# Performance work log

Hardware: AMD Instinct MI355X
Metric: run time of the kernel (lower is better)

The kernel has to match this reference:

```python
import jax, jax.numpy as jnp
import numpy as np

D = 256       # d_model
HEADS = 8     # n_heads
PTS = 4       # n_points
FF = 1024     # dim_feedforward
HD = D // HEADS
B, Q = 8, 900
HH, WW = 100, 100


def setup_inputs() -> dict:
    key = jax.random.key(0)
    ks = iter(jax.random.split(key, 40))
    p = lambda shape: jax.random.normal(next(ks), shape, dtype=jnp.float32) * 0.02
    inp = {
        "tgt": jax.random.normal(next(ks), (B, Q, D), dtype=jnp.float32),
        "memory": jax.random.normal(next(ks), (B, HH * WW, D), dtype=jnp.float32),
        "H": HH,
        "W": WW,
        # self-attention (nn.MultiheadAttention) params
        "in_proj_w": p((3 * D, D)), "in_proj_b": p((3 * D,)),
        "out_proj_w": p((D, D)), "out_proj_b": p((D,)),
        # layer norms
        "norm1_s": jnp.ones((D,)), "norm1_b": jnp.zeros((D,)),
        "norm2_s": jnp.ones((D,)), "norm2_b": jnp.zeros((D,)),
        "norm3_s": jnp.ones((D,)), "norm3_b": jnp.zeros((D,)),
        # deformable cross-attention params
        "vproj_w": p((D, D)), "vproj_b": p((D,)),
        "offs_w": p((HEADS * PTS * 2, D)), "offs_b": p((HEADS * PTS * 2,)),
        "attw_w": p((HEADS * PTS, D)), "attw_b": p((HEADS * PTS,)),
        "ref_w": p((2, D)), "ref_b": p((2,)),
        "cout_w": p((D, D)), "cout_b": p((D,)),
        # FFN params
        "ffn_w1": p((FF, D)), "ffn_b1": p((FF,)),
        "ffn_w2": p((D, FF)), "ffn_b2": p((D,)),
    }
    return inp


def _layer_norm(x, s, b):
    m = jnp.mean(x, -1, keepdims=True)
    v = jnp.mean((x - m) ** 2, -1, keepdims=True)
    return (x - m) * jax.lax.rsqrt(v + 1e-5) * s + b


def _mha(x, wi, bi, wo, bo):
    b, q, _ = x.shape
    qkv = x @ wi.T + bi
    qh, kh, vh = jnp.split(qkv, 3, axis=-1)
    qh = qh.reshape(b, q, HEADS, HD).transpose(0, 2, 1, 3)
    kh = kh.reshape(b, q, HEADS, HD).transpose(0, 2, 1, 3)
    vh = vh.reshape(b, q, HEADS, HD).transpose(0, 2, 1, 3)
    att = jax.nn.softmax(jnp.einsum('bhqd,bhkd->bhqk', qh, kh) / np.float32(np.sqrt(HD)), axis=-1)
    o = jnp.einsum('bhqk,bhkd->bhqd', att, vh).transpose(0, 2, 1, 3).reshape(b, q, D)
    return o @ wo.T + bo


def _deform_attn(q, mem, H, W, vproj_w, vproj_b, offs_w, offs_b, attw_w, attw_b,
                 ref_w, ref_b, cout_w, cout_b):
    b, nq, _ = q.shape
    # per-query normalized reference points (x, y) in [0,1]
    ref = jax.nn.sigmoid(q @ ref_w.T + ref_b)                         # [B,Q,2]
    offs = (q @ offs_w.T + offs_b).reshape(b, nq, HEADS, PTS, 2)      # [B,Q,h,p,2]
    attw = jax.nn.softmax((q @ attw_w.T + attw_b).reshape(b, nq, HEADS, PTS), axis=-1)
    val = (mem @ vproj_w.T + vproj_b).reshape(b, H * W, HEADS, HD).transpose(0, 2, 1, 3)  # [B,h,HW,hd]
    wh = jnp.array([W, H], dtype=q.dtype)
    loc = ref[:, :, None, None, :] + offs / wh                        # normalized sampling loc
    x = loc[..., 0] * W - 0.5                                         # pixel coords (align_corners=False)
    y = loc[..., 1] * H - 0.5
    x0 = jnp.floor(x); y0 = jnp.floor(y)
    lx = x - x0; ly = y - y0
    x0i = x0.astype(jnp.int32); y0i = y0.astype(jnp.int32)

    def gather(xi, yi):
        valid = ((xi >= 0) & (xi < W) & (yi >= 0) & (yi < H)).astype(q.dtype)
        idx = jnp.clip(yi, 0, H - 1) * W + jnp.clip(xi, 0, W - 1)     # [B,Q,h,p]
        idxt = idx.transpose(0, 2, 1, 3).reshape(b, HEADS, nq * PTS, 1)
        g = jnp.take_along_axis(val, idxt, axis=2)                    # [B,h,Q*p,hd]
        g = g.reshape(b, HEADS, nq, PTS, HD).transpose(0, 2, 1, 3, 4)  # [B,Q,h,p,hd]
        return g * valid[..., None]

    samp = (gather(x0i, y0i) * ((1 - lx) * (1 - ly))[..., None]
            + gather(x0i + 1, y0i) * (lx * (1 - ly))[..., None]
            + gather(x0i, y0i + 1) * ((1 - lx) * ly)[..., None]
            + gather(x0i + 1, y0i + 1) * (lx * ly)[..., None])        # [B,Q,h,p,hd]
    out = jnp.sum(samp * attw[..., None], axis=3).reshape(b, nq, D)
    return out @ cout_w.T + cout_b


def reference(tgt, memory, H, W, in_proj_w, in_proj_b, out_proj_w, out_proj_b,
              norm1_s, norm1_b, norm2_s, norm2_b, norm3_s, norm3_b,
              vproj_w, vproj_b, offs_w, offs_b, attw_w, attw_b, ref_w, ref_b,
              cout_w, cout_b, ffn_w1, ffn_b1, ffn_w2, ffn_b2):
    t2 = _mha(tgt, in_proj_w, in_proj_b, out_proj_w, out_proj_b)
    t = _layer_norm(tgt + t2, norm1_s, norm1_b)
    t2 = _deform_attn(t, memory, H, W, vproj_w, vproj_b, offs_w, offs_b,
                      attw_w, attw_b, ref_w, ref_b, cout_w, cout_b)
    t = _layer_norm(t + t2, norm2_s, norm2_b)
    f = jnp.maximum(t @ ffn_w1.T + ffn_b1, 0) @ ffn_w2.T + ffn_b2
    return _layer_norm(t + f, norm3_s, norm3_b)
```

## Files before the change

### kernel.cpp

```cpp
#include <hip/hip_runtime.h>
#include <hip/hip_bf16.h>

typedef __hip_bfloat16 bf16;
typedef __attribute__((ext_vector_type(8))) short short8;
typedef __attribute__((ext_vector_type(4))) float f32x4;

#define BB 8
#define QQ 900
#define DD 256
#define NH 8
#define HD 32
#define NPTS 4
#define FFD 1024
#define HH 100
#define WW2 100
#define HWTOT 10000

#define QT 64
#define KTC 128
#define NCHUNK ((QQ + KTC - 1) / KTC)
#define QB 4
#define VTP 1024

__device__ inline float tofloat(float x) { return x; }
__device__ inline float tofloat(bf16 x) { return __bfloat162float(x); }
__device__ inline float bf2f(unsigned short u) {
    return __uint_as_float(((unsigned int)u) << 16);
}
__device__ inline void storev(bf16* p, float v) { *p = __float2bfloat16(v); }
__device__ inline void storev(float* p, float v) { *p = v; }

__device__ inline void load4(const float* p, float* v) {
    const float4 t = *(const float4*)p;
    v[0] = t.x; v[1] = t.y; v[2] = t.z; v[3] = t.w;
}
__device__ inline void load4(const bf16* p, float* v) {
    const ushort4 t = *(const ushort4*)p;
    v[0] = bf2f(t.x); v[1] = bf2f(t.y); v[2] = bf2f(t.z); v[3] = bf2f(t.w);
}
__device__ inline void store4(float* p, const float* v) {
    float4 t = {v[0], v[1], v[2], v[3]};
    *(float4*)p = t;
}
__device__ inline void store4(bf16* p, const float* v) {
    bf16 t[4] = {__float2bfloat16(v[0]), __float2bfloat16(v[1]),
                 __float2bfloat16(v[2]), __float2bfloat16(v[3])};
    *(uint2*)p = *(const uint2*)t;
}
__device__ inline void cvt4(const float* s, bf16* d) {
    float v[4];
    load4(s, v);
    store4(d, v);
}

typedef __attribute__((address_space(1))) const unsigned int gas_u32;
typedef __attribute__((address_space(3))) unsigned int las_u32;
__device__ inline void gload_lds16(const bf16* g, bf16* l) {
    __builtin_amdgcn_global_load_lds(
        (gas_u32*)(unsigned long long)(const void*)g,
        (las_u32*)(unsigned int)(unsigned long long)(const void*)l, 16, 0, 0);
}

__global__ void pack_kernel(const float* __restrict__ in_proj_w, const float* __restrict__ out_proj_w,
                            const float* __restrict__ cout_w, const float* __restrict__ ffn_w1,
                            const float* __restrict__ ffn_w2, const float* __restrict__ vproj_w,
                            const float* __restrict__ offs_w, const float* __restrict__ attw_w,
                            const float* __restrict__ ref_w, const float* __restrict__ offs_b,
                            const float* __restrict__ attw_b, const float* __restrict__ ref_b,
                            const float* __restrict__ tgt, bf16* __restrict__ wpk,
                            bf16* __restrict__ tgtb, float* __restrict__ dbias,
                            bf16* __restrict__ vt) {
    const int i4 = (blockIdx.x * 256 + threadIdx.x) * 4;
    const int TOT = 950272 + 1843200 + 128 + 2097152;
    if (i4 >= TOT) return;
    if (i4 < 196608) {
        cvt4(in_proj_w + i4, wpk + i4);
    } else if (i4 < 262144) {
        cvt4(out_proj_w + (i4 - 196608), wpk + i4);
    } else if (i4 < 327680) {
        cvt4(cout_w + (i4 - 262144), wpk + i4);
    } else if (i4 < 589824) {
        cvt4(ffn_w1 + (i4 - 327680), wpk + i4);
    } else if (i4 < 851968) {
        cvt4(ffn_w2 + (i4 - 589824), wpk + i4);
    } else if (i4 < 917504) {
        cvt4(vproj_w + (i4 - 851968), wpk + i4);
    } else if (i4 < 950272) {
#pragma unroll
        for (int j = 0; j < 4; ++j) {
            const int jj = i4 + j - 917504;
            const int r = jj >> 8, c = jj & 255;
            float v = 0.f;
            if (r < 64) v = offs_w[r * 256 + c];
            else if (r < 96) v = attw_w[(r - 64) * 256 + c];
            else if (r < 98) v = ref_w[(r - 96) * 256 + c];
            wpk[i4 + j] = __float2bfloat16(v);
        }
    } else if (i4 < 950272 + 1843200) {
        cvt4(tgt + (i4 - 950272), tgtb + (i4 - 950272));
    } else if (i4 < 950272 + 1843200 + 128) {
#pragma unroll
        for (int j = 0; j < 4; ++j) {
            const int jj = i4 + j - (950272 + 1843200);
            float v = 0.f;
            if (jj < 64) v = offs_b[jj];
            else if (jj < 96) v = attw_b[jj - 64];
            else if (jj < 98) v = ref_b[jj - 96];
            dbias[jj] = v;
        }
    } else {
        const uint2 z = {0u, 0u};
        *(uint2*)&vt[i4 - (950272 + 1843200 + 128)] = z;
    }
}

template <int BM, int BN, int BK, int ACT, int VT, typename OT>
__global__ __launch_bounds__(256) void gemm_v6(const bf16* __restrict__ A,
                                               const bf16* __restrict__ W,
                                               const float* __restrict__ bias,
                                               OT* __restrict__ C, bf16* __restrict__ vt,
                                               int M, int N, int K) {
    constexpr int MACC = BM / 32;
    constexpr int NACC = BN / 32;
    constexpr int KK = BK / 32;
    constexpr int P = BK / 8;
    constexpr int CA = (BM * BK) / 8 / 256;
    constexpr int CB = (BN * BK) / 8 / 256;
    __shared__ bf16 As[2][BM * BK];
    __shared__ bf16 Bs[2][BN * BK];
    const int bm = blockIdx.y * BM, bn = blockIdx.x * BN;
    const int tid = threadIdx.x;
    const int lane = tid & 63, wave = tid >> 6;
    const int l15 = lane & 15, g = lane >> 4;
    const int wr = wave & 1, wc = wave >> 1;
    auto swz = [](int row) { return (P == 8) ? (row & 7) : ((row >> 1) & 3); };
    const f32x4 zf = {0.f, 0.f, 0.f, 0.f};
    f32x4 acc[MACC][NACC];
#pragma unroll
    for (int mi = 0; mi < MACC; ++mi)
#pragma unroll
        for (int ni = 0; ni < NACC; ++ni) acc[mi][ni] = zf;

    const int NT = K / BK;
    int cur = 0;

    {
#pragma unroll
        for (int i = 0; i < CA; ++i) {
            const int slot = i * 256 + wave * 64 + lane;
            const int row = slot / P, pc = slot % P;
            const int gp = pc ^ swz(row);
            const int grow = min(bm + row, M - 1);
            gload_lds16(A + (size_t)grow * K + 0 + gp * 8,
                        &As[0][(i * 256 + wave * 64) * 8]);
        }
#pragma unroll
        for (int i = 0; i < CB; ++i) {
            const int slot = i * 256 + wave * 64 + lane;
            const int row = slot / P, pc = slot % P;
            const int gp = pc ^ swz(row);
            gload_lds16(W + (size_t)(bn + row) * K + 0 + gp * 8,
                        &Bs[0][(i * 256 + wave * 64) * 8]);
        }
    }
    __syncthreads();

    for (int t = 0; t < NT; ++t) {
        if (t + 1 < NT) {
            const int k0 = (t + 1) * BK;
#pragma unroll
            for (int i = 0; i < CA; ++i) {
                const int slot = i * 256 + wave * 64 + lane;
                const int row = slot / P, pc = slot % P;
                const int gp = pc ^ swz(row);
                const int grow = min(bm + row, M - 1);
                gload_lds16(A + (size_t)grow * K + k0 + gp * 8,
                            &As[cur ^ 1][(i * 256 + wave * 64) * 8]);
            }
#pragma unroll
            for (int i = 0; i < CB; ++i) {
                const int slot = i * 256 + wave * 64 + lane;
                const int row = slot / P, pc = slot % P;
                const int gp = pc ^ swz(row);
                gload_lds16(W + (size_t)(bn + row) * K + k0 + gp * 8,
                            &Bs[cur ^ 1][(i * 256 + wave * 64) * 8]);
            }
        }
#pragma unroll
        for (int kk = 0; kk < KK; ++kk) {
            short8 af[MACC];
#pragma unroll
            for (int mi = 0; mi < MACC; ++mi) {
                const int row = wr * (BM / 2) + mi * 16 + l15;
                const int byte = row * (2 * BK) + (((kk * 4 + g) ^ swz(row)) << 4);
                af[mi] = *(const short8*)((const char*)&As[cur][0] + byte);
            }
#pragma unroll
            for (int ni = 0; ni < NACC; ++ni) {
                const int col = wc * (BN / 2) + ni * 16 + l15;
                const int byte = col * (2 * BK) + (((kk * 4 + g) ^ swz(col)) << 4);
                const short8 bfv = *(const short8*)((const char*)&Bs[cur][0] + byte);
#pragma unroll
                for (int mi = 0; mi < MACC; ++mi)
                    acc[mi][ni] = __builtin_amdgcn_mfma_f32_16x16x32_bf16(af[mi], bfv,
                                                                          acc[mi][ni], 0, 0, 0);
            }
        }
        __syncthreads();
        cur ^= 1;
    }

#pragma unroll
    for (int ni = 0; ni < NACC; ++ni) {
        const int col = bn + wc * (BN / 2) + ni * 16 + l15;
        const float bv = bias[col];
#pragma unroll
        for (int mi = 0; mi < MACC; ++mi) {
            const int row0 = bm + wr * (BM / 2) + mi * 16 + g * 4;
            if (VT && col >= 512) {
                if (row0 < M) {
                    const int b = row0 / 900, q = row0 % 900;
                    const int hd = col - 512;
                    bf16 u4[4];
#pragma unroll
                    for (int r = 0; r < 4; ++r) u4[r] = __float2bfloat16(acc[mi][ni][r] + bv);
                    *(uint2*)&vt[((size_t)(b * NH + (hd >> 5)) * HD + (hd & 31)) * VTP + q] =
                        *(const uint2*)u4;
                }
            } else {
#pragma unroll
                for (int r = 0; r < 4; ++r) {
                    const int row = row0 + r;
                    if (row < M) {
                        float v = acc[mi][ni][r] + bv;
                        if (ACT == 1) v = fmaxf(v, 0.f);
                        if (VT)
                            storev((bf16*)C + (size_t)row * 512 + col, v);
                        else
                            storev(&C[(size_t)row * N + col], v);
                    }
                }
            }
        }
    }
}

__global__ __launch_bounds__(256) void mha_mfma_kernel(const bf16* __restrict__ qkv,
                                                       const bf16* __restrict__ vt,
                                                       bf16* __restrict__ o) {
    const int qt = blockIdx.x, h = blockIdx.y, b = blockIdx.z;
    const int tid = threadIdx.x;
    const int lane = tid & 63, wave = tid >> 6;
    const int l15 = lane & 15, g = lane >> 4;
    __shared__ bf16 KP[4096];
    __shared__ bf16 Vls[4096];
    __shared__ bf16 Pls[4][16][136];
    const size_t base = (size_t)b * QQ * 512;
    const bf16* vbase = vt + (size_t)(b * NH + h) * HD * VTP;
    const int q0 = qt * QT;

    short8 qa = {0, 0, 0, 0, 0, 0, 0, 0};
    {
        const int qg = q0 + wave * 16 + l15;
        if (qg < QQ)
            qa = *(const short8*)(qkv + base + (size_t)qg * 512 + h * HD + g * 8);
    }
    f32x4 accO[2] = {{0.f, 0.f, 0.f, 0.f}, {0.f, 0.f, 0.f, 0.f}};
    float l_acc[4] = {0.f, 0.f, 0.f, 0.f};
    const float sl2e = 0.17677669529663687f * 1.4426950408889634f;

    for (int c = 0; c < NCHUNK; ++c) {
        const int k0 = c * KTC;
        __syncthreads();
#pragma unroll
        for (int i = 0; i < 2; ++i) {
            const int r = (wave * 2 + i) * 16 + (lane >> 2);
            const int p = lane & 3;
            const int gp = p ^ ((r >> 1) & 3);
            const int kg = min(k0 + r, QQ - 1);
            gload_lds16(qkv + base + (size_t)kg * 512 + 256 + h * HD + gp * 8,
                        &KP[(wave * 2 + i) * 512]);
        }
#pragma unroll
        for (int i = 0; i < 2; ++i) {
            const int s = (wave * 2 + i) * 64 + lane;
            const int vrow = s >> 4, vp = s & 15;
            const int gp = vp ^ (vrow & 7);
            gload_lds16(vbase + (size_t)vrow * VTP + k0 + gp * 8, &Vls[(wave * 2 + i) * 512]);
        }
        __syncthreads();

        f32x4 s[8];
#pragma unroll
        for (int t = 0; t < 8; ++t) {
            const int row = t * 16 + l15;
            const short8 kb = *(const short8*)&KP[row * 32 + (g ^ ((row >> 1) & 3)) * 8];
            const f32x4 z = {0.f, 0.f, 0.f, 0.f};
            s[t] = __builtin_amdgcn_mfma_f32_16x16x32_bf16(qa, kb, z, 0, 0, 0);
        }
#pragma unroll
        for (int t = 0; t < 8; ++t) {
            const bool cv = (k0 + t * 16 + l15) < QQ;
#pragma unroll
            for (int r = 0; r < 4; ++r) {
                const float p = cv ? exp2f(s[t][r] * sl2e) : 0.f;
                l_acc[r] += p;
                Pls[wave][g * 4 + r][t * 16 + l15] = __float2bfloat16(p);
            }
        }
#pragma unroll
        for (int s4 = 0; s4 < 4; ++s4) {
            const short8 pa = *(const short8*)&Pls[wave][l15][s4 * 32 + g * 8];
#pragma unroll
            for (int t2 = 0; t2 < 2; ++t2) {
                const int vrow = t2 * 16 + l15;
                const int pp = (s4 * 4 + g) ^ (vrow & 7);
                const short8 vb = *(const short8*)&Vls[vrow * 128 + pp * 8];
                accO[t2] = __builtin_amdgcn_mfma_f32_16x16x32_bf16(pa, vb, accO[t2], 0, 0, 0);
            }
        }
    }
#pragma unroll
    for (int r = 0; r < 4; ++r) {
        float l = l_acc[r];
        l += __shfl_xor(l, 1);
        l += __shfl_xor(l, 2);
        l += __shfl_xor(l, 4);
        l += __shfl_xor(l, 8);
        const int row = q0 + wave * 16 + g * 4 + r;
        if (row < QQ) {
            const float inv = 1.f / l;
#pragma unroll
            for (int t2 = 0; t2 < 2; ++t2) {
                storev(&o[((size_t)b * QQ + row) * DD + h * HD + t2 * 16 + l15],
                       accO[t2][r] * inv);
            }
        }
    }
}

template <typename TR, typename TO>
__global__ __launch_bounds__(256) void add_ln_kernel(const TR* __restrict__ resid,
                                                     const bf16* __restrict__ y,
                                                     const float* __restrict__ g,
                                                     const float* __restrict__ bta,
                                                     TO* __restrict__ out) {
    const int tid = threadIdx.x;
    const int lane = tid & 63, wave = tid >> 6;
    const int row = blockIdx.x * 4 + wave;
    const int c0 = lane * 4;
    const size_t base = (size_t)row * DD + c0;
    float v[4], yv[4];
    load4(resid + base, v);
    load4(y + base, yv);
#pragma unroll
    for (int j = 0; j < 4; ++j) v[j] += yv[j];
    float s = v[0] + v[1] + v[2] + v[3];
    s += __shfl_xor(s, 1);  s += __shfl_xor(s, 2);  s += __shfl_xor(s, 4);
    s += __shfl_xor(s, 8);  s += __shfl_xor(s, 16); s += __shfl_xor(s, 32);
    const float mean = s * (1.f / DD);
    float d[4];
    float q = 0.f;
#pragma unroll
    for (int j = 0; j < 4; ++j) {
        d[j] = v[j] - mean;
        q += d[j] * d[j];
    }
    q += __shfl_xor(q, 1);  q += __shfl_xor(q, 2);  q += __shfl_xor(q, 4);
    q += __shfl_xor(q, 8);  q += __shfl_xor(q, 16); q += __shfl_xor(q, 32);
    const float rstd = rsqrtf(q * (1.f / DD) + 1e-5f);
    float gv[4], bv[4], ov[4];
    load4(g + c0, gv);
    load4(bta + c0, bv);
#pragma unroll
    for (int j = 0; j < 4; ++j) ov[j] = d[j] * rstd * gv[j] + bv[j];
    store4(out + base, ov);
}

__global__ __launch_bounds__(256) void deform_gather_kernel(
    const float* __restrict__ dots, const float* __restrict__ mem,
    bf16* __restrict__ G, float* __restrict__ wsumg) {
    const int qt = blockIdx.x, b = blockIdx.y;
    const int tid = threadIdx.x;
    const int q0 = qt * QB;
    __shared__ int sidx[QB][32][4];
    __shared__ float swt[QB][32][4];

    if (tid < 128) {
        const int q = tid >> 5, hp = tid & 31;
        const float* dr = dots + ((size_t)b * QQ + q0 + q) * 128;
        const float ox = dr[hp * 2], oy = dr[hp * 2 + 1];
        float ad = dr[64 + hp];
        const float rx = dr[96], ry = dr[97];
        float mx = ad;
        mx = fmaxf(mx, __shfl_xor(mx, 1));
        mx = fmaxf(mx, __shfl_xor(mx, 2));
        float e = __expf(ad - mx);
        float sm = e;
        sm += __shfl_xor(sm, 1);
        sm += __shfl_xor(sm, 2);
        const float a = e / sm;
        const float refx = 1.f / (1.f + __expf(-rx));
        const float refy = 1.f / (1.f + __expf(-ry));
        const float x = (refx + ox * (1.f / WW2)) * WW2 - 0.5f;
        const float y = (refy + oy * (1.f / HH)) * HH - 0.5f;
        const float x0f = floorf(x), y0f = floorf(y);
        const float lx = x - x0f, ly = y - y0f;
        const int x0 = (int)x0f, y0 = (int)y0f;
        const float cw[4] = {(1 - lx) * (1 - ly), lx * (1 - ly), (1 - lx) * ly, lx * ly};
        const int cx[4] = {x0, x0 + 1, x0, x0 + 1};
        const int cy[4] = {y0, y0, y0 + 1, y0 + 1};
        float cs = 0.f;
#pragma unroll
        for (int cc = 0; cc < 4; ++cc) {
            const bool valid = cx[cc] >= 0 && cx[cc] < WW2 && cy[cc] >= 0 && cy[cc] < HH;
            const int xi = min(max(cx[cc], 0), WW2 - 1);
            const int yi = min(max(cy[cc], 0), HH - 1);
            sidx[q][hp][cc] = yi * WW2 + xi;
            const float w = valid ? a * cw[cc] : 0.f;
            swt[q][hp][cc] = w;
            cs += w;
        }
        cs += __shfl_xor(cs, 1);
        cs += __shfl_xor(cs, 2);
        if ((hp & 3) == 0) wsumg[((size_t)b * QQ + q0 + q) * NH + (hp >> 2)] = cs;
    }
    __syncthreads();

    {
        const int q = tid >> 6, cbase = (tid & 63) * 4;
        const float* mb = mem + (size_t)b * HWTOT * DD;
        bf16* gq = G + ((size_t)(b * QQ + q0 + q) * NH) * DD + cbase;
#pragma unroll
        for (int h = 0; h < NH; ++h) {
            float4 acc = {0.f, 0.f, 0.f, 0.f};
#pragma unroll
            for (int p = 0; p < NPTS; ++p) {
                const int hp = h * NPTS + p;
                const int4 ix = *(const int4*)sidx[q][hp];
                const float4 wt = *(const float4*)swt[q][hp];
                const float4 v0 = *(const float4*)(mb + (size_t)ix.x * DD + cbase);
                const float4 v1 = *(const float4*)(mb + (size_t)ix.y * DD + cbase);
                const float4 v2 = *(const float4*)(mb + (size_t)ix.z * DD + cbase);
                const float4 v3 = *(const float4*)(mb + (size_t)ix.w * DD + cbase);
                acc.x += wt.x * v0.x + wt.y * v1.x + wt.z * v2.x + wt.w * v3.x;
                acc.y += wt.x * v0.y + wt.y * v1.y + wt.z * v2.y + wt.w * v3.y;
                acc.z += wt.x * v0.z + wt.y * v1.z + wt.z * v2.z + wt.w * v3.z;
                acc.w += wt.x * v0.w + wt.y * v1.w + wt.z * v2.w + wt.w * v3.w;
            }
            bf16 out4[4] = {__float2bfloat16(acc.x), __float2bfloat16(acc.y),
                            __float2bfloat16(acc.z), __float2bfloat16(acc.w)};
            *(uint2*)(gq + (size_t)h * DD) = *(const uint2*)out4;
        }
    }
}

__global__ __launch_bounds__(256) void gemm_vproj_kernel(
    const bf16* __restrict__ G, const bf16* __restrict__ Wv,
    const float* __restrict__ vb, const float* __restrict__ wsumg,
    bf16* __restrict__ samp, int M) {
    __shared__ unsigned short As[64][40];
    __shared__ unsigned short Bs[32][40];
    const int h = blockIdx.x, bm = blockIdx.y * 64;
    const int tid = threadIdx.x;
    const int lane = tid & 63, wave = tid >> 6;
    const int l15 = lane & 15, g = lane >> 4;
    const int sr = tid >> 2, sc = (tid & 3) * 8;
    f32x4 acc[2] = {{0.f, 0.f, 0.f, 0.f}, {0.f, 0.f, 0.f, 0.f}};
    const uint4 zero4 = {0u, 0u, 0u, 0u};
    for (int k0 = 0; k0 < DD; k0 += 32) {
        __syncthreads();
        {
            const int arow = bm + sr;
            uint4 a4 = (arow < M)
                ? *(const uint4*)(G + ((size_t)arow * NH + h) * DD + k0 + sc)
                : zero4;
            *(uint4*)&As[sr][sc] = a4;
            if (sr < 32) {
                uint4 b4 = *(const uint4*)(Wv + (size_t)(h * 32 + sr) * DD + k0 + sc);
                *(uint4*)&Bs[sr][sc] = b4;
            }
        }
        __syncthreads();
        const short8 af = *(const short8*)&As[wave * 16 + l15][g * 8];
#pragma unroll
        for (int ct = 0; ct < 2; ++ct) {
            const short8 bf = *(const short8*)&Bs[ct * 16 + l15][g * 8];
            acc[ct] = __builtin_amdgcn_mfma_f32_16x16x32_bf16(af, bf, acc[ct], 0, 0, 0);
        }
    }
#pragma unroll
    for (int ct = 0; ct < 2; ++ct) {
        const int col = h * 32 + ct * 16 + l15;
        const float bv = vb[col];
#pragma unroll
        for (int r = 0; r < 4; ++r) {
            const int row = bm + wave * 16 + g * 4 + r;
            if (row < M) {
                const float v = acc[ct][r] + bv * wsumg[(size_t)row * NH + h];
                storev(&samp[(size_t)row * DD + col], v);
            }
        }
    }
}

extern "C" void kernel_launch(void* const* d_in, const int* in_sizes, int n_in,
                              void* d_out, int out_size, void* d_ws, size_t ws_size,
                              hipStream_t stream) {
    const float* tgt = (const float*)d_in[0];
    const float* memory = (const float*)d_in[1];
    const float* in_proj_w = (const float*)d_in[4];
    const float* in_proj_b = (const float*)d_in[5];
    const float* out_proj_w = (const float*)d_in[6];
    const float* out_proj_b = (const float*)d_in[7];
    const float* norm1_s = (const float*)d_in[8];
    const float* norm1_b = (const float*)d_in[9];
    const float* norm2_s = (const float*)d_in[10];
    const float* norm2_b = (const float*)d_in[11];
    const float* norm3_s = (const float*)d_in[12];
    const float* norm3_b = (const float*)d_in[13];
    const float* vproj_w = (const float*)d_in[14];
    const float* vproj_b = (const float*)d_in[15];
    const float* offs_w = (const float*)d_in[16];
    const float* offs_b = (const float*)d_in[17];
    const float* attw_w = (const float*)d_in[18];
    const float* attw_b = (const float*)d_in[19];
    const float* ref_w = (const float*)d_in[20];
    const float* ref_b = (const float*)d_in[21];
    const float* cout_w = (const float*)d_in[22];
    const float* cout_b = (const float*)d_in[23];
    const float* ffn_w1 = (const float*)d_in[24];
    const float* ffn_b1 = (const float*)d_in[25];
    const float* ffn_w2 = (const float*)d_in[26];
    const float* ffn_b2 = (const float*)d_in[27];

    const int M = BB * QQ;
    bf16* ws = (bf16*)d_ws;
    size_t off = 0;
    bf16* qkv = ws + off;  off += (size_t)M * 512;
    bf16* o = ws + off;    off += (size_t)M * DD;
    bf16* t1 = ws + off;   off += (size_t)M * DD;
    bf16* tmp = ws + off;  off += (size_t)M * DD;
    bf16* ffh = ws + off;  off += (size_t)M * FFD;
    bf16* tgtb = ws + off; off += (size_t)M * DD;
    bf16* wpk = ws + off;  off += 950272;
    float* dbias = (float*)(ws + off); off += 256;
    float* wsumg = (float*)(ws + off); off += (size_t)M * NH * 2;
    bf16* Gws = ws + off;  off += (size_t)M * NH * DD;
    bf16* vt = ws + off;   off += (size_t)BB * NH * HD * VTP;
    bf16* samp = o;
    bf16* t2n = qkv;
    float* dots = (float*)ffh;

    bf16* w_in = wpk;
    bf16* w_out = wpk + 196608;
    bf16* w_cout = wpk + 262144;
    bf16* w_ffn1 = wpk + 327680;
    bf16* w_ffn2 = wpk + 589824;
    bf16* w_vproj = wpk + 851968;
    bf16* w_dots = wpk + 917504;

    const int MT = (M + 63) / 64;
    const int LNB = M / 4;
    const int TOT = 950272 + 1843200 + 128 + 2097152;

    pack_kernel<<<(TOT / 4 + 255) / 256, 256, 0, stream>>>(
        in_proj_w, out_proj_w, cout_w, ffn_w1, ffn_w2, vproj_w, offs_w, attw_w, ref_w,
        offs_b, attw_b, ref_b, tgt, wpk, tgtb, dbias, vt);
    gemm_v6<64, 128, 32, 0, 1, bf16><<<dim3(6, MT), 256, 0, stream>>>(tgtb, w_in, in_proj_b,
                                                                      qkv, vt, M, 768, DD);
    mha_mfma_kernel<<<dim3((QQ + QT - 1) / QT, NH, BB), 256, 0, stream>>>(qkv, vt, o);
    gemm_v6<64, 64, 64, 0, 0, bf16><<<dim3(4, MT), 256, 0, stream>>>(o, w_out, out_proj_b,
                                                                     tmp, nullptr, M, DD, DD);
    add_ln_kernel<float, bf16><<<LNB, 256, 0, stream>>>(tgt, tmp, norm1_s, norm1_b, t1);
    gemm_v6<64, 64, 64, 0, 0, float><<<dim3(2, MT), 256, 0, stream>>>(t1, w_dots, dbias,
                                                                      dots, nullptr, M, 128, DD);
    deform_gather_kernel<<<dim3(QQ / QB, BB), 256, 0, stream>>>(dots, memory, Gws, wsumg);
    gemm_vproj_kernel<<<dim3(NH, MT), 256, 0, stream>>>(Gws, w_vproj, vproj_b, wsumg,
                                                        samp, M);
    gemm_v6<64, 64, 64, 0, 0, bf16><<<dim3(4, MT), 256, 0, stream>>>(samp, w_cout, cout_b,
                                                                     tmp, nullptr, M, DD, DD);
    add_ln_kernel<bf16, bf16><<<LNB, 256, 0, stream>>>(t1, tmp, norm2_s, norm2_b, t2n);
    gemm_v6<64, 128, 32, 1, 0, bf16><<<dim3(8, MT), 256, 0, stream>>>(t2n, w_ffn1, ffn_b1,
                                                                      ffh, nullptr, M, FFD, DD);
    gemm_v6<64, 64, 64, 0, 0, bf16><<<dim3(4, MT), 256, 0, stream>>>(ffh, w_ffn2, ffn_b2,
                                                                     tmp, nullptr, M, DD, FFD);
    add_ln_kernel<bf16, float><<<LNB, 256, 0, stream>>>(t2n, tmp, norm3_s, norm3_b,
                                                        (float*)d_out);
}
```

Measured before the change: 320.8 us.

## Double-buffer LDS tiles with async global-to-LDS loads in MHA and vproj GEMM

The MHA kernel now double-buffers its K and V tiles in LDS and prefetches the next chunk with async global-to-LDS loads while computing on the current one, dropping one barrier per iteration. The vproj GEMM kernel is restructured the same way: K-step goes from 32 to 64, tiles are loaded through async LDS loads into XOR-swizzled double buffers, and waves are rearranged into a 2x2 layout. This is meant to hide global-load latency behind MFMA work at the cost of more LDS per block, which could lower occupancy. The vproj kernel now clamps out-of-range rows instead of zero-filling them. There also appears to be no explicit wait for the async loads before the barrier, which may or may not be sufficient.

```diff
diff --git a/kernel.cpp b/kernel.cpp
--- a/kernel.cpp
+++ b/kernel.cpp
@@ -252,12 +252,16 @@
     const int tid = threadIdx.x;
     const int lane = tid & 63, wave = tid >> 6;
     const int l15 = lane & 15, g = lane >> 4;
-    __shared__ bf16 KP[4096];
-    __shared__ bf16 Vls[4096];
+    __shared__ bf16 KP[2][4096];
+    __shared__ bf16 Vls[2][4096];
     __shared__ bf16 Pls[4][16][136];
     const size_t base = (size_t)b * QQ * 512;
     const bf16* vbase = vt + (size_t)(b * NH + h) * HD * VTP;
     const int q0 = qt * QT;
+
+    const int k_r = (wave * 2) * 16 + (lane >> 2);
+    const int k_gp = (lane & 3);
+    const int v_s0 = (wave * 2) * 64 + lane;
 
     short8 qa = {0, 0, 0, 0, 0, 0, 0, 0};
     {
@@ -269,32 +273,50 @@
     float l_acc[4] = {0.f, 0.f, 0.f, 0.f};
     const float sl2e = 0.17677669529663687f * 1.4426950408889634f;
 
+#pragma unroll
+    for (int i = 0; i < 2; ++i) {
+        const int r = k_r + i * 16;
+        const int gp = k_gp ^ ((r >> 1) & 3);
+        const int kg = min(r, QQ - 1);
+        gload_lds16(qkv + base + (size_t)kg * 512 + 256 + h * HD + gp * 8,
+                    &KP[0][(wave * 2 + i) * 512]);
+    }
+#pragma unroll
+    for (int i = 0; i < 2; ++i) {
+        const int s = v_s0 + i * 64;
+        const int vrow = s >> 4, vp = s & 15;
+        const int gp = vp ^ (vrow & 7);
+        gload_lds16(vbase + (size_t)vrow * VTP + 0 + gp * 8, &Vls[0][(wave * 2 + i) * 512]);
+    }
+    __syncthreads();
+
+    int cur = 0;
     for (int c = 0; c < NCHUNK; ++c) {
+        if (c + 1 < NCHUNK) {
+            const int k0n = (c + 1) * KTC;
+#pragma unroll
+            for (int i = 0; i < 2; ++i) {
+                const int r = k_r + i * 16;
+                const int gp = k_gp ^ ((r >> 1) & 3);
+                const int kg = min(k0n + r, QQ - 1);
+                gload_lds16(qkv + base + (size_t)kg * 512 + 256 + h * HD + gp * 8,
+                            &KP[cur ^ 1][(wave * 2 + i) * 512]);
+            }
+#pragma unroll
+            for (int i = 0; i < 2; ++i) {
+                const int s = v_s0 + i * 64;
+                const int vrow = s >> 4, vp = s & 15;
+                const int gp = vp ^ (vrow & 7);
+                gload_lds16(vbase + (size_t)vrow * VTP + k0n + gp * 8,
+                            &Vls[cur ^ 1][(wave * 2 + i) * 512]);
+            }
+        }
         const int k0 = c * KTC;
-        __syncthreads();
-#pragma unroll
-        for (int i = 0; i < 2; ++i) {
-            const int r = (wave * 2 + i) * 16 + (lane >> 2);
-            const int p = lane & 3;
-            const int gp = p ^ ((r >> 1) & 3);
-            const int kg = min(k0 + r, QQ - 1);
-            gload_lds16(qkv + base + (size_t)kg * 512 + 256 + h * HD + gp * 8,
-                        &KP[(wave * 2 + i) * 512]);
-        }
-#pragma unroll
-        for (int i = 0; i < 2; ++i) {
-            const int s = (wave * 2 + i) * 64 + lane;
-            const int vrow = s >> 4, vp = s & 15;
-            const int gp = vp ^ (vrow & 7);
-            gload_lds16(vbase + (size_t)vrow * VTP + k0 + gp * 8, &Vls[(wave * 2 + i) * 512]);
-        }
-        __syncthreads();
-
         f32x4 s[8];
 #pragma unroll
         for (int t = 0; t < 8; ++t) {
             const int row = t * 16 + l15;
-            const short8 kb = *(const short8*)&KP[row * 32 + (g ^ ((row >> 1) & 3)) * 8];
+            const short8 kb = *(const short8*)&KP[cur][row * 32 + (g ^ ((row >> 1) & 3)) * 8];
             const f32x4 z = {0.f, 0.f, 0.f, 0.f};
             s[t] = __builtin_amdgcn_mfma_f32_16x16x32_bf16(qa, kb, z, 0, 0, 0);
         }
@@ -315,10 +337,12 @@
             for (int t2 = 0; t2 < 2; ++t2) {
                 const int vrow = t2 * 16 + l15;
                 const int pp = (s4 * 4 + g) ^ (vrow & 7);
-                const short8 vb = *(const short8*)&Vls[vrow * 128 + pp * 8];
+                const short8 vb = *(const short8*)&Vls[cur][vrow * 128 + pp * 8];
                 accO[t2] = __builtin_amdgcn_mfma_f32_16x16x32_bf16(pa, vb, accO[t2], 0, 0, 0);
             }
         }
+        __syncthreads();
+        cur ^= 1;
     }
 #pragma unroll
     for (int r = 0; r < 4; ++r) {
@@ -459,45 +483,87 @@
     const bf16* __restrict__ G, const bf16* __restrict__ Wv,
     const float* __restrict__ vb, const float* __restrict__ wsumg,
     bf16* __restrict__ samp, int M) {
-    __shared__ unsigned short As[64][40];
-    __shared__ unsigned short Bs[32][40];
+    __shared__ bf16 As[2][64 * 64];
+    __shared__ bf16 Bs[2][32 * 64];
     const int h = blockIdx.x, bm = blockIdx.y * 64;
+    const bf16* A = G + (size_t)h * DD;
+    const bf16* W = Wv + (size_t)h * 32 * DD;
     const int tid = threadIdx.x;
     const int lane = tid & 63, wave = tid >> 6;
     const int l15 = lane & 15, g = lane >> 4;
-    const int sr = tid >> 2, sc = (tid & 3) * 8;
-    f32x4 acc[2] = {{0.f, 0.f, 0.f, 0.f}, {0.f, 0.f, 0.f, 0.f}};
-    const uint4 zero4 = {0u, 0u, 0u, 0u};
-    for (int k0 = 0; k0 < DD; k0 += 32) {
+    const int wr = wave & 1, wc = wave >> 1;
+    const f32x4 zf = {0.f, 0.f, 0.f, 0.f};
+    f32x4 acc[2] = {zf, zf};
+
+    const int NT = DD / 64;
+    int cur = 0;
+    {
+#pragma unroll
+        for (int i = 0; i < 2; ++i) {
+            const int slot = i * 256 + wave * 64 + lane;
+            const int row = slot >> 3, pc = slot & 7;
+            const int gp = pc ^ (row & 7);
+            const int grow = min(bm + row, M - 1);
+            gload_lds16(A + (size_t)grow * 2048 + 0 + gp * 8,
+                        &As[0][(i * 256 + wave * 64) * 8]);
+        }
+        {
+            const int slot = wave * 64 + lane;
+            const int row = slot >> 3, pc = slot & 7;
+            const int gp = pc ^ (row & 7);
+            gload_lds16(W + (size_t)row * DD + 0 + gp * 8, &Bs[0][(wave * 64) * 8]);
+        }
+    }
+    __syncthreads();
+
+    for (int t = 0; t < NT; ++t) {
+        if (t + 1 < NT) {
+            const int k0 = (t + 1) * 64;
+#pragma unroll
+            for (int i = 0; i < 2; ++i) {
+                const int slot = i * 256 + wave * 64 + lane;
+                const int row = slot >> 3, pc = slot & 7;
+                const int gp = pc ^ (row & 7);
+                const int grow = min(bm + row, M - 1);
+                gload_lds16(A + (size_t)grow * 2048 + k0 + gp * 8,
+                            &As[cur ^ 1][(i * 256 + wave * 64) * 8]);
+            }
+            {
+                const int slot = wave * 64 + lane;
+                const int row = slot >> 3, pc = slot & 7;
+                const int gp = pc ^ (row & 7);
+                gload_lds16(W + (size_t)row * DD + k0 + gp * 8, &Bs[cur ^ 1][(wave * 64) * 8]);
+            }
+        }
+#pragma unroll
+        for (int kk = 0; kk < 2; ++kk) {
+            short8 af[2];
+#pragma unroll
+            for (int mi = 0; mi < 2; ++mi) {
+                const int row = wr * 32 + mi * 16 + l15;
+                const int byte = row * 128 + (((kk * 4 + g) ^ (row & 7)) << 4);
+                af[mi] = *(const short8*)((const char*)&As[cur][0] + byte);
+            }
+            const int col = wc * 16 + l15;
+            const int byte = col * 128 + (((kk * 4 + g) ^ (col & 7)) << 4);
+            const short8 bfv = *(const short8*)((const char*)&Bs[cur][0] + byte);
+#pragma unroll
+            for (int mi = 0; mi < 2; ++mi)
+                acc[mi] = __builtin_amdgcn_mfma_f32_16x16x32_bf16(af[mi], bfv, acc[mi], 0, 0, 0);
+        }
         __syncthreads();
-        {
-            const int arow = bm + sr;
-            uint4 a4 = (arow < M)
-                ? *(const uint4*)(G + ((size_t)arow * NH + h) * DD + k0 + sc)
-                : zero4;
-            *(uint4*)&As[sr][sc] = a4;
-            if (sr < 32) {
-                uint4 b4 = *(const uint4*)(Wv + (size_t)(h * 32 + sr) * DD + k0 + sc);
-                *(uint4*)&Bs[sr][sc] = b4;
-            }
-        }
-        __syncthreads();
-        const short8 af = *(const short8*)&As[wave * 16 + l15][g * 8];
-#pragma unroll
-        for (int ct = 0; ct < 2; ++ct) {
-            const short8 bf = *(const short8*)&Bs[ct * 16 + l15][g * 8];
-            acc[ct] = __builtin_amdgcn_mfma_f32_16x16x32_bf16(af, bf, acc[ct], 0, 0, 0);
-        }
-    }
-#pragma unroll
-    for (int ct = 0; ct < 2; ++ct) {
-        const int col = h * 32 + ct * 16 + l15;
-        const float bv = vb[col];
+        cur ^= 1;
+    }
+
+    const int col = h * 32 + wc * 16 + l15;
+    const float bv = vb[col];
+#pragma unroll
+    for (int mi = 0; mi < 2; ++mi) {
 #pragma unroll
         for (int r = 0; r < 4; ++r) {
-            const int row = bm + wave * 16 + g * 4 + r;
+            const int row = bm + wr * 32 + mi * 16 + g * 4 + r;
             if (row < M) {
-                const float v = acc[ct][r] + bv * wsumg[(size_t)row * NH + h];
+                const float v = acc[mi][r] + bv * wsumg[(size_t)row * NH + h];
                 storev(&samp[(size_t)row * DD + col], v);
             }
         }
```

Result: no change. 319.6 us (-0.4%).
